# Kernel tuning notes

Measured on AMD Instinct MI355X. Metric: run time of the kernel, lower is better.

The kernel has to match this reference:

```python
import jax, jax.numpy as jnp
import numpy as np

T = 32        # time_step
H = 64        # n_hidden (and dense width)
A = 8         # nb_actions
OBS_DIM = 512
B = 4096      # sequences; obs rows = B*T
LN_EPS = 1e-12  # tf.contrib.layers.layer_norm epsilon


def setup_inputs() -> dict:
    key = jax.random.key(0)
    ks = jax.random.split(key, 10)
    s = 0.1
    return {
        "obs":  jax.random.normal(ks[0], (B * T, OBS_DIM), jnp.float32),
        "W0":   jax.random.normal(ks[1], (OBS_DIM, H), jnp.float32) * s,
        "b0":   jnp.zeros((H,), jnp.float32),
        "gamma": jnp.ones((H,), jnp.float32),
        "beta":  jnp.zeros((H,), jnp.float32),
        "Wfw":  jax.random.normal(ks[2], (2 * H, 4 * H), jnp.float32) * s,
        "bfw":  jnp.zeros((4 * H,), jnp.float32),
        "Wbw":  jax.random.normal(ks[3], (2 * H, 4 * H), jnp.float32) * s,
        "bbw":  jnp.zeros((4 * H,), jnp.float32),
        "Wc":   jax.random.uniform(ks[4], (H, A), jnp.float32, -0.003, 0.003),
        "bc":   jnp.zeros((A,), jnp.float32),
    }


def _lstm_scan(xs, W, b):
    """BasicLSTMCell (forget_bias=1.0). xs: [T, B, H] -> hs: [T, B, H]."""
    nb = xs.shape[1]
    init = (jnp.zeros((nb, H), xs.dtype), jnp.zeros((nb, H), xs.dtype))

    def step(carry, x_t):
        c, h = carry
        z = jnp.concatenate([x_t, h], axis=-1) @ W + b  # [B, 4H]
        i, j, f, o = jnp.split(z, 4, axis=-1)           # TF gate order i,j,f,o
        c = c * jax.nn.sigmoid(f + 1.0) + jax.nn.sigmoid(i) * jnp.tanh(j)
        h = jnp.tanh(c) * jax.nn.sigmoid(o)
        return (c, h), h

    _, hs = jax.lax.scan(step, init, xs)
    return hs


def reference(obs, W0, b0, gamma, beta, Wfw, bfw, Wbw, bbw, Wc, bc):
    # dense(64) + layer_norm + relu
    x = obs @ W0 + b0                                   # [B*T, H]
    mu = jnp.mean(x, axis=-1, keepdims=True)
    var = jnp.mean(jnp.square(x - mu), axis=-1, keepdims=True)
    x = gamma * (x - mu) / jnp.sqrt(var + LN_EPS) + beta
    x = jax.nn.relu(x)

    xt = x.reshape(-1, T, H).transpose(1, 0, 2)          # [T, B, H]
    hs_fw = _lstm_scan(xt, Wfw, bfw)                     # [T, B, H]
    hs_bw = _lstm_scan(xt[::-1], Wbw, bbw)[::-1]         # reverse-in, reverse-out

    # tf.reshape on the (fw, bw) tuple stacks along a new leading axis:
    # [2, B, T, H] -> [2B, T*H, 1]; conv1d(kernel=stride=H) == per-step proj.
    y = jnp.stack([hs_fw.transpose(1, 0, 2), hs_bw.transpose(1, 0, 2)], axis=0)
    y = y.reshape(-1, T, H)                              # [2B, T, H]
    out = jnp.tanh(jnp.einsum('btk,ka->bta', y, Wc) + bc)  # [2B, T, A]
    return out
```

## Files before the change

kernel.cpp:

```cpp
#include <hip/hip_runtime.h>
#include <hip/hip_bf16.h>

typedef __attribute__((ext_vector_type(8))) short bf16x8;
typedef __attribute__((ext_vector_type(4))) float f32x4;

#define MFMA_BF16 __builtin_amdgcn_mfma_f32_16x16x32_bf16

__device__ __forceinline__ unsigned pk2(float a, float b) {
  __hip_bfloat162 t = __float22bfloat162_rn(make_float2(a, b));
  return *reinterpret_cast<unsigned*>(&t);
}
__device__ __forceinline__ unsigned short f2bf_hw(float f) {
  __hip_bfloat16 h = __float2bfloat16(f);
  return *reinterpret_cast<unsigned short*>(&h);
}
__device__ __forceinline__ float sigm(float x) {
  return __builtin_amdgcn_rcpf(1.f + __expf(-x));
}
__device__ __forceinline__ float tanh_f(float x) {
  return 1.f - 2.f * __builtin_amdgcn_rcpf(1.f + __expf(2.f * x));
}

__global__ void k0_conv(const float* __restrict__ W0, const float* __restrict__ Wfw,
                        const float* __restrict__ Wbw, unsigned short* __restrict__ wfrag,
                        unsigned short* __restrict__ wlstm) {
  int gid = blockIdx.x * 256 + threadIdx.x;
  if (gid < 4096) {
    int f = gid >> 6, l = gid & 63;
    int k0 = (f >> 2) * 32 + ((l >> 4) << 3);
    int n = (f & 3) * 16 + (l & 15);
    bf16x8 v;
#pragma unroll
    for (int j = 0; j < 8; ++j) v[j] = (short)f2bf_hw(W0[(k0 + j) * 64 + n]);
    *(bf16x8*)(wfrag + gid * 8) = v;
  } else if (gid < 12288) {
    int g2 = gid - 4096;
    const float* W = (g2 < 4096) ? Wfw : Wbw;
    int f = (g2 & 4095) >> 6, l = g2 & 63;
    int wv = f >> 4, gate = (f >> 2) & 3, kf = f & 3;
    int col = gate * 64 + wv * 16 + (l & 15);
    int kr = kf * 32 + ((l >> 4) << 3);
    bf16x8 v;
#pragma unroll
    for (int j = 0; j < 8; ++j) v[j] = (short)f2bf_hw(W[(kr + j) * 256 + col]);
    *(bf16x8*)(wlstm + g2 * 8) = v;
  }
}

__global__ __launch_bounds__(256, 2) void k_dense_ln(
    const float* __restrict__ obs, const unsigned short* __restrict__ wfrag,
    const float* __restrict__ b0, const float* __restrict__ gam,
    const float* __restrict__ bet, unsigned short* __restrict__ xout) {
  __shared__ unsigned short xs[4096];
  const int tid = threadIdx.x, w = tid >> 6, l = tid & 63;
  const int g = l >> 4, c = l & 15;
  const long rb = (long)blockIdx.x * 64 + w * 16;

  float b0v[4], gv[4], bv[4];
#pragma unroll
  for (int nt = 0; nt < 4; ++nt) {
    int col = nt * 16 + c;
    b0v[nt] = b0[col]; gv[nt] = gam[col]; bv[nt] = bet[col];
  }

  const float* arow = obs + (rb + c) * 512 + g * 8;
  const unsigned short* wfl = wfrag + l * 8;

  f32x4 acc[4];
#pragma unroll
  for (int nt = 0; nt < 4; ++nt) acc[nt] = (f32x4){0.f, 0.f, 0.f, 0.f};

  float4 a0 = *(const float4*)(arow);
  float4 a1 = *(const float4*)(arow + 4);
  bf16x8 Bc[4];
#pragma unroll
  for (int nt = 0; nt < 4; ++nt) Bc[nt] = *(const bf16x8*)(wfl + nt * 512);

#pragma unroll
  for (int kf = 0; kf < 16; ++kf) {
    union { bf16x8 v; unsigned u[4]; } af;
    af.u[0] = pk2(a0.x, a0.y); af.u[1] = pk2(a0.z, a0.w);
    af.u[2] = pk2(a1.x, a1.y); af.u[3] = pk2(a1.z, a1.w);
    float4 n0, n1;
    bf16x8 Bn[4];
    if (kf < 15) {
      n0 = *(const float4*)(arow + (kf + 1) * 32);
      n1 = *(const float4*)(arow + (kf + 1) * 32 + 4);
#pragma unroll
      for (int nt = 0; nt < 4; ++nt)
        Bn[nt] = *(const bf16x8*)(wfl + ((kf + 1) * 4 + nt) * 512);
    }
#pragma unroll
    for (int nt = 0; nt < 4; ++nt)
      acc[nt] = MFMA_BF16(af.v, Bc[nt], acc[nt], 0, 0, 0);
    if (kf < 15) {
      a0 = n0; a1 = n1;
#pragma unroll
      for (int nt = 0; nt < 4; ++nt) Bc[nt] = Bn[nt];
    }
  }

  float vv[4][4], s1[4], s2[4];
#pragma unroll
  for (int r = 0; r < 4; ++r) { s1[r] = 0.f; s2[r] = 0.f; }
#pragma unroll
  for (int nt = 0; nt < 4; ++nt)
#pragma unroll
    for (int r = 0; r < 4; ++r) {
      float val = acc[nt][r] + b0v[nt];
      vv[nt][r] = val; s1[r] += val; s2[r] += val * val;
    }
#pragma unroll
  for (int r = 0; r < 4; ++r) {
#pragma unroll
    for (int m = 1; m <= 8; m <<= 1) {
      s1[r] += __shfl_xor(s1[r], m);
      s2[r] += __shfl_xor(s2[r], m);
    }
  }
  unsigned short* xw = xs + w * 1024;
#pragma unroll
  for (int r = 0; r < 4; ++r) {
    float mu = s1[r] * 0.015625f;
    float var = s2[r] * 0.015625f - mu * mu;
    float inv = rsqrtf(var + 1e-12f);
    int row = g * 4 + r;
#pragma unroll
    for (int nt = 0; nt < 4; ++nt) {
      float xn = (vv[nt][r] - mu) * inv * gv[nt] + bv[nt];
      xw[(row * 64 + nt * 16 + c) ^ (g << 3)] = f2bf_hw(fmaxf(xn, 0.f));
    }
  }
#pragma unroll
  for (int m2 = 0; m2 < 2; ++m2) {
    int m = m2 * 64 + l;
    int row = m >> 3, u8 = m & 7;
    bf16x8 v = *(const bf16x8*)(xw + ((row * 64 + u8 * 8) ^ ((row >> 2) << 3)));
    *(bf16x8*)(xout + (rb + row) * 64 + u8 * 8) = v;
  }
}

__global__ __launch_bounds__(256, 2) void k_lstm(
    const unsigned short* __restrict__ x, const unsigned short* __restrict__ wlstm,
    const float* __restrict__ bfw, const float* __restrict__ bbw,
    const float* __restrict__ Wc, const float* __restrict__ bc,
    float* __restrict__ out) {
  __shared__ unsigned short xr[4 * 1024];
  __shared__ unsigned short hl[2 * 1024];
  const int tid = threadIdx.x, w = tid >> 6, l = tid & 63;
  const int g = l >> 4, c = l & 15;
  const int dir = blockIdx.x >> 8;
  const int sq = (blockIdx.x & 255) * 16;
  const float* bias = dir ? bbw : bfw;

  bf16x8 Bf[4][4];
  const unsigned short* wl = wlstm + ((long)dir * 4096 + w * 16 * 64) * 8;
#pragma unroll
  for (int gate = 0; gate < 4; ++gate)
#pragma unroll
    for (int kf = 0; kf < 4; ++kf)
      Bf[gate][kf] = *(const bf16x8*)(wl + ((gate * 4 + kf) * 64 + l) * 8);
  float bz[4];
#pragma unroll
  for (int gate = 0; gate < 4; ++gate) bz[gate] = bias[gate * 64 + w * 16 + c];

  bf16x8 Pc[2];
#pragma unroll
  for (int kf = 0; kf < 2; ++kf)
#pragma unroll
    for (int j = 0; j < 8; ++j) Pc[kf][j] = 0;
  float bcv = 0.f;
  if (w == 0 && c < 8) {
#pragma unroll
    for (int kf = 0; kf < 2; ++kf)
#pragma unroll
      for (int j = 0; j < 8; ++j)
        Pc[kf][j] = (short)f2bf_hw(Wc[(kf * 32 + g * 8 + j) * 8 + c]);
    bcv = bc[c];
  }

  const int sRow = tid >> 4, uc = tid & 15;
  const unsigned short* xg = x + ((long)(sq + sRow) * 32) * 64 + uc * 4;
  const unsigned xdst = ((unsigned)(((uc >> 3) * 64 + ((uc >> 1) & 3) * 16 + sRow) * 16 +
                                    (uc & 1) * 8));

  {
    int te0 = dir ? 31 : 0, te1 = dir ? 30 : 1;
    uint2 v0 = *(const uint2*)(xg + te0 * 64);
    uint2 v1 = *(const uint2*)(xg + te1 * 64);
    *(uint2*)((char*)xr + 0 * 2048 + xdst) = v0;
    *(uint2*)((char*)xr + 1 * 2048 + xdst) = v1;
  }
  for (int i = tid; i < 512; i += 256) ((unsigned*)hl)[i] = 0u;
  float cs[4] = {0.f, 0.f, 0.f, 0.f};
  __syncthreads();

  const int hq = w >> 1;
  const int hgp = ((w & 1) * 2 + (c >> 3)) * 16;
  const int hlo = c & 7;

  int p = 0;
  for (int t = 0; t < 32; ++t) {
    const int te = dir ? 31 - t : t;
    uint2 pf;
    const bool do_pf = (t + 2 < 32);
    if (do_pf) {
      int tep = dir ? 29 - t : t + 2;
      pf = *(const uint2*)(xg + tep * 64);
    }

    const char* xs = (const char*)xr + (t & 3) * 2048;
    bf16x8 Ax0 = *(const bf16x8*)(xs + l * 16);
    bf16x8 Ax1 = *(const bf16x8*)(xs + 1024 + l * 16);
    bf16x8 Ah0 = *(const bf16x8*)((const char*)hl + p * 2048 + l * 16);
    bf16x8 Ah1 = *(const bf16x8*)((const char*)hl + p * 2048 + 1024 + l * 16);

    f32x4 acc[4];
#pragma unroll
    for (int gate = 0; gate < 4; ++gate)
      acc[gate] = (f32x4){bz[gate], bz[gate], bz[gate], bz[gate]};
#pragma unroll
    for (int gate = 0; gate < 4; ++gate) {
      acc[gate] = MFMA_BF16(Ax0, Bf[gate][0], acc[gate], 0, 0, 0);
      acc[gate] = MFMA_BF16(Ax1, Bf[gate][1], acc[gate], 0, 0, 0);
      acc[gate] = MFMA_BF16(Ah0, Bf[gate][2], acc[gate], 0, 0, 0);
      acc[gate] = MFMA_BF16(Ah1, Bf[gate][3], acc[gate], 0, 0, 0);
    }

    const int wb = (p ^ 1) * 1024;
#pragma unroll
    for (int r = 0; r < 4; ++r) {
      float si = sigm(acc[0][r]);
      float tj = tanh_f(acc[1][r]);
      float sf = sigm(acc[2][r] + 1.f);
      float so = sigm(acc[3][r]);
      cs[r] = cs[r] * sf + si * tj;
      hl[wb + (hq * 64 + hgp + 4 * g + r) * 8 + hlo] = f2bf_hw(tanh_f(cs[r]) * so);
    }
    if (do_pf) *(uint2*)((char*)xr + ((t + 2) & 3) * 2048 + xdst) = pf;
    __syncthreads();

    if (w == 0 && t >= 1) {
      f32x4 pa = (f32x4){0.f, 0.f, 0.f, 0.f};
      pa = MFMA_BF16(Ah0, Pc[0], pa, 0, 0, 0);
      pa = MFMA_BF16(Ah1, Pc[1], pa, 0, 0, 0);
      if (c < 8) {
        int tp = dir ? 32 - t : t - 1;
#pragma unroll
        for (int r = 0; r < 4; ++r) {
          long orow = (long)dir * 4096 + sq + 4 * g + r;
          out[(orow * 32 + tp) * 8 + c] = tanh_f(pa[r] + bcv);
        }
      }
    }
    p ^= 1;
  }

  if (w == 0) {
    bf16x8 Ph0 = *(const bf16x8*)((const char*)hl + p * 2048 + l * 16);
    bf16x8 Ph1 = *(const bf16x8*)((const char*)hl + p * 2048 + 1024 + l * 16);
    f32x4 pa = (f32x4){0.f, 0.f, 0.f, 0.f};
    pa = MFMA_BF16(Ph0, Pc[0], pa, 0, 0, 0);
    pa = MFMA_BF16(Ph1, Pc[1], pa, 0, 0, 0);
    if (c < 8) {
      int tp = dir ? 0 : 31;
#pragma unroll
      for (int r = 0; r < 4; ++r) {
        long orow = (long)dir * 4096 + sq + 4 * g + r;
        out[(orow * 32 + tp) * 8 + c] = tanh_f(pa[r] + bcv);
      }
    }
  }
}

extern "C" void kernel_launch(void* const* d_in, const int* in_sizes, int n_in,
                              void* d_out, int out_size, void* d_ws, size_t ws_size,
                              hipStream_t stream) {
  const float* obs = (const float*)d_in[0];
  const float* W0  = (const float*)d_in[1];
  const float* b0  = (const float*)d_in[2];
  const float* gam = (const float*)d_in[3];
  const float* bet = (const float*)d_in[4];
  const float* Wfw = (const float*)d_in[5];
  const float* bfw = (const float*)d_in[6];
  const float* Wbw = (const float*)d_in[7];
  const float* bbw = (const float*)d_in[8];
  const float* Wc  = (const float*)d_in[9];
  const float* bc  = (const float*)d_in[10];
  float* out = (float*)d_out;

  unsigned short* wfrag = (unsigned short*)d_ws;
  unsigned short* wlstm = wfrag + 4096 * 8;
  unsigned short* xbf   = wlstm + 8192 * 8;

  k0_conv<<<48, 256, 0, stream>>>(W0, Wfw, Wbw, wfrag, wlstm);
  k_dense_ln<<<2048, 256, 0, stream>>>(obs, wfrag, b0, gam, bet, xbf);
  k_lstm<<<512, 256, 0, stream>>>(xbf, wlstm, bfw, bbw, Wc, bc, out);
}
```

Measured before the change: 106.0 us.

## Stage obs and LSTM inputs via global_load_lds with explicit vmcnt pipelining

The dense+LN kernel now streams obs tiles into a double-buffered 64KB LDS region with direct global-to-LDS loads (swizzled) and explicit vmcnt waits, instead of per-thread register prefetch. The LSTM kernel preloads all 32 timesteps of its x slice into LDS up front via global_load_lds. It then replaces __syncthreads with manual waitcnt plus s_barrier, where the owning wave waits only for the timestep it loaded, and fully unrolls the time loop. This is meant to hide global latency and remove register-staging overhead. In exchange, 64KB of LDS per block lowers occupancy, and the hand-counted vmcnt values are fragile.

```diff
diff --git a/kernel.cpp b/kernel.cpp
--- a/kernel.cpp
+++ b/kernel.cpp
@@ -5,6 +5,11 @@
 typedef __attribute__((ext_vector_type(4))) float f32x4;
 
 #define MFMA_BF16 __builtin_amdgcn_mfma_f32_16x16x32_bf16
+
+#define GLDS16(gp, lp)                                                        \
+  __builtin_amdgcn_global_load_lds(                                           \
+      (const __attribute__((address_space(1))) void*)(gp),                    \
+      (__attribute__((address_space(3))) void*)(lp), 16, 0, 0)
 
 __device__ __forceinline__ unsigned pk2(float a, float b) {
   __hip_bfloat162 t = __float22bfloat162_rn(make_float2(a, b));
@@ -51,10 +56,11 @@
     const float* __restrict__ obs, const unsigned short* __restrict__ wfrag,
     const float* __restrict__ b0, const float* __restrict__ gam,
     const float* __restrict__ bet, unsigned short* __restrict__ xout) {
-  __shared__ unsigned short xs[4096];
+  __shared__ __align__(16) char lds[65536];
   const int tid = threadIdx.x, w = tid >> 6, l = tid & 63;
   const int g = l >> 4, c = l & 15;
-  const long rb = (long)blockIdx.x * 64 + w * 16;
+  const long blk64 = (long)blockIdx.x * 64;
+  const long rb = blk64 + w * 16;
 
   float b0v[4], gv[4], bv[4];
 #pragma unroll
@@ -62,41 +68,61 @@
     int col = nt * 16 + c;
     b0v[nt] = b0[col]; gv[nt] = gam[col]; bv[nt] = bet[col];
   }
-
-  const float* arow = obs + (rb + c) * 512 + g * 8;
   const unsigned short* wfl = wfrag + l * 8;
 
+  const int sr0 = w * 16 + (l >> 5);
+  const int su = l & 31;
+  const char* gB = (const char*)obs + blk64 * 2048;
+
+  asm volatile("s_waitcnt vmcnt(0)" ::: "memory");
+
+#define K1_STAGE(q)                                                           \
+  {                                                                           \
+    _Pragma("unroll") for (int i = 0; i < 8; ++i) {                           \
+      int r_ = sr0 + 2 * i;                                                   \
+      int chk_ = su ^ (r_ & 7);                                               \
+      const char* gp_ = gB + (long)r_ * 2048 + (q) * 512 + chk_ * 16;         \
+      char* lp_ = lds + ((q) & 1) * 32768 + (w * 512 + i * 64) * 16;          \
+      GLDS16(gp_, lp_);                                                       \
+    }                                                                         \
+  }
+
+  K1_STAGE(0);
+  K1_STAGE(1);
+
   f32x4 acc[4];
 #pragma unroll
   for (int nt = 0; nt < 4; ++nt) acc[nt] = (f32x4){0.f, 0.f, 0.f, 0.f};
 
-  float4 a0 = *(const float4*)(arow);
-  float4 a1 = *(const float4*)(arow + 4);
-  bf16x8 Bc[4];
-#pragma unroll
-  for (int nt = 0; nt < 4; ++nt) Bc[nt] = *(const bf16x8*)(wfl + nt * 512);
-
-#pragma unroll
-  for (int kf = 0; kf < 16; ++kf) {
-    union { bf16x8 v; unsigned u[4]; } af;
-    af.u[0] = pk2(a0.x, a0.y); af.u[1] = pk2(a0.z, a0.w);
-    af.u[2] = pk2(a1.x, a1.y); af.u[3] = pk2(a1.z, a1.w);
-    float4 n0, n1;
-    bf16x8 Bn[4];
-    if (kf < 15) {
-      n0 = *(const float4*)(arow + (kf + 1) * 32);
-      n1 = *(const float4*)(arow + (kf + 1) * 32 + 4);
-#pragma unroll
-      for (int nt = 0; nt < 4; ++nt)
-        Bn[nt] = *(const bf16x8*)(wfl + ((kf + 1) * 4 + nt) * 512);
-    }
-#pragma unroll
-    for (int nt = 0; nt < 4; ++nt)
-      acc[nt] = MFMA_BF16(af.v, Bc[nt], acc[nt], 0, 0, 0);
-    if (kf < 15) {
-      a0 = n0; a1 = n1;
-#pragma unroll
-      for (int nt = 0; nt < 4; ++nt) Bc[nt] = Bn[nt];
+#pragma unroll
+  for (int q = 0; q < 4; ++q) {
+    if (q < 3) asm volatile("s_waitcnt vmcnt(8)" ::: "memory");
+    else       asm volatile("s_waitcnt vmcnt(0)" ::: "memory");
+    __builtin_amdgcn_s_barrier();
+    __builtin_amdgcn_sched_barrier(0);
+
+    const char* bufb = lds + (q & 1) * 32768 + (w * 16 + c) * 512;
+#pragma unroll
+    for (int kf2 = 0; kf2 < 4; ++kf2) {
+      bf16x8 B0 = *(const bf16x8*)(wfl + ((q * 4 + kf2) * 4 + 0) * 512);
+      bf16x8 B1 = *(const bf16x8*)(wfl + ((q * 4 + kf2) * 4 + 1) * 512);
+      bf16x8 B2 = *(const bf16x8*)(wfl + ((q * 4 + kf2) * 4 + 2) * 512);
+      bf16x8 B3 = *(const bf16x8*)(wfl + ((q * 4 + kf2) * 4 + 3) * 512);
+      int v0 = kf2 * 8 + g * 2;
+      float4 f0 = *(const float4*)(bufb + ((v0 + 0) ^ (c & 7)) * 16);
+      float4 f1 = *(const float4*)(bufb + ((v0 + 1) ^ (c & 7)) * 16);
+      union { bf16x8 v; unsigned u[4]; } af;
+      af.u[0] = pk2(f0.x, f0.y); af.u[1] = pk2(f0.z, f0.w);
+      af.u[2] = pk2(f1.x, f1.y); af.u[3] = pk2(f1.z, f1.w);
+      acc[0] = MFMA_BF16(af.v, B0, acc[0], 0, 0, 0);
+      acc[1] = MFMA_BF16(af.v, B1, acc[1], 0, 0, 0);
+      acc[2] = MFMA_BF16(af.v, B2, acc[2], 0, 0, 0);
+      acc[3] = MFMA_BF16(af.v, B3, acc[3], 0, 0, 0);
+    }
+    if (q < 2) {
+      __builtin_amdgcn_s_barrier();
+      __builtin_amdgcn_sched_barrier(0);
+      K1_STAGE(q + 2);
     }
   }
 
@@ -118,7 +144,7 @@
       s2[r] += __shfl_xor(s2[r], m);
     }
   }
-  unsigned short* xw = xs + w * 1024;
+  unsigned short* xw = (unsigned short*)lds + w * 1024;
 #pragma unroll
   for (int r = 0; r < 4; ++r) {
     float mu = s1[r] * 0.015625f;
@@ -145,7 +171,7 @@
     const float* __restrict__ bfw, const float* __restrict__ bbw,
     const float* __restrict__ Wc, const float* __restrict__ bc,
     float* __restrict__ out) {
-  __shared__ unsigned short xr[4 * 1024];
+  __shared__ __align__(16) char xl[65536];
   __shared__ unsigned short hl[2 * 1024];
   const int tid = threadIdx.x, w = tid >> 6, l = tid & 63;
   const int g = l >> 4, c = l & 15;
@@ -179,39 +205,42 @@
     bcv = bc[c];
   }
 
-  const int sRow = tid >> 4, uc = tid & 15;
-  const unsigned short* xg = x + ((long)(sq + sRow) * 32) * 64 + uc * 4;
-  const unsigned xdst = ((unsigned)(((uc >> 3) * 64 + ((uc >> 1) & 3) * 16 + sRow) * 16 +
-                                    (uc & 1) * 8));
-
-  {
-    int te0 = dir ? 31 : 0, te1 = dir ? 30 : 1;
-    uint2 v0 = *(const uint2*)(xg + te0 * 64);
-    uint2 v1 = *(const uint2*)(xg + te1 * 64);
-    *(uint2*)((char*)xr + 0 * 2048 + xdst) = v0;
-    *(uint2*)((char*)xr + 1 * 2048 + xdst) = v1;
-  }
-  for (int i = tid; i < 512; i += 256) ((unsigned*)hl)[i] = 0u;
+  asm volatile("s_waitcnt vmcnt(0)" ::: "memory");
+
+  const int ss = l >> 3, sc = l & 7;
+#pragma unroll
+  for (int j = 0; j < 8; ++j) {
+    int tt = w * 8 + j;
+    int te = dir ? 31 - tt : tt;
+#pragma unroll
+    for (int p = 0; p < 2; ++p) {
+      int s = p * 8 + ss;
+      const char* gp = (const char*)x +
+          ((long)(sq + s) * 32 + te) * 128 + (long)(sc ^ (s & 7)) * 16;
+      char* lp = xl + tt * 2048 + p * 1024;
+      GLDS16(gp, lp);
+    }
+  }
+
+  for (int i = tid; i < 1024; i += 256) ((unsigned*)hl)[i] = 0u;
   float cs[4] = {0.f, 0.f, 0.f, 0.f};
-  __syncthreads();
+
+  if (w == 0) asm volatile("s_waitcnt vmcnt(14)" ::: "memory");
+  asm volatile("s_waitcnt lgkmcnt(0)" ::: "memory");
+  __builtin_amdgcn_s_barrier();
+  __builtin_amdgcn_sched_barrier(0);
 
   const int hq = w >> 1;
   const int hgp = ((w & 1) * 2 + (c >> 3)) * 16;
   const int hlo = c & 7;
 
   int p = 0;
+#pragma unroll
   for (int t = 0; t < 32; ++t) {
     const int te = dir ? 31 - t : t;
-    uint2 pf;
-    const bool do_pf = (t + 2 < 32);
-    if (do_pf) {
-      int tep = dir ? 29 - t : t + 2;
-      pf = *(const uint2*)(xg + tep * 64);
-    }
-
-    const char* xs = (const char*)xr + (t & 3) * 2048;
-    bf16x8 Ax0 = *(const bf16x8*)(xs + l * 16);
-    bf16x8 Ax1 = *(const bf16x8*)(xs + 1024 + l * 16);
+    const char* xt = xl + t * 2048 + c * 128;
+    bf16x8 Ax0 = *(const bf16x8*)(xt + (long)((g) ^ (c & 7)) * 16);
+    bf16x8 Ax1 = *(const bf16x8*)(xt + (long)((4 + g) ^ (c & 7)) * 16);
     bf16x8 Ah0 = *(const bf16x8*)((const char*)hl + p * 2048 + l * 16);
     bf16x8 Ah1 = *(const bf16x8*)((const char*)hl + p * 2048 + 1024 + l * 16);
 
@@ -237,8 +266,14 @@
       cs[r] = cs[r] * sf + si * tj;
       hl[wb + (hq * 64 + hgp + 4 * g + r) * 8 + hlo] = f2bf_hw(tanh_f(cs[r]) * so);
     }
-    if (do_pf) *(uint2*)((char*)xr + ((t + 2) & 3) * 2048 + xdst) = pf;
-    __syncthreads();
+
+    if (t + 1 < 32) {
+      if (w == ((t + 1) >> 3))
+        asm volatile("s_waitcnt vmcnt(%0)" :: "i"(14 - 2 * ((t + 1) & 7)) : "memory");
+    }
+    asm volatile("s_waitcnt lgkmcnt(0)" ::: "memory");
+    __builtin_amdgcn_s_barrier();
+    __builtin_amdgcn_sched_barrier(0);
 
     if (w == 0 && t >= 1) {
       f32x4 pa = (f32x4){0.f, 0.f, 0.f, 0.f};
```

Result: faster. 103.9 us (-2.0%).
